# Performance work log

Measured on AMD Instinct MI355X. Metric: run time of the kernel, lower is better.

## Reference

```python
import jax, jax.numpy as jnp
import numpy as np

DIM = 1024
N_HEADS = 16
D_K = DIM // N_HEADS
B, N = 2, 2048


def _pairwise_dist(p):
    # p: [B, N, 3] -> Euclidean cdist [B, N, N], grad-safe at zero distance
    sq = jnp.sum(p * p, axis=-1)                      # [B, N]
    d2 = sq[:, :, None] + sq[:, None, :] - 2.0 * jnp.einsum('bnd,bmd->bnm', p, p)
    d2 = jnp.maximum(d2, 0.0)
    safe = jnp.where(d2 > 0.0, d2, 1.0)
    return jnp.where(d2 > 0.0, jnp.sqrt(safe), 0.0)


def setup_inputs() -> dict:
    key = jax.random.key(0)
    ks = jax.random.split(key, 11)
    s = 1.0 / np.sqrt(DIM)
    inp = {
        'x': jax.random.normal(ks[0], (B, N, DIM), jnp.float32),
        'positions': jax.random.normal(ks[1], (B, N, 3), jnp.float32),
        'W_q': jax.random.normal(ks[2], (DIM, DIM), jnp.float32) * s,
        'b_q': jnp.zeros((DIM,), jnp.float32),
        'W_k': jax.random.normal(ks[3], (DIM, DIM), jnp.float32) * s,
        'b_k': jnp.zeros((DIM,), jnp.float32),
        'W_v': jax.random.normal(ks[4], (DIM, DIM), jnp.float32) * s,
        'b_v': jnp.zeros((DIM,), jnp.float32),
        'W_o': jax.random.normal(ks[5], (DIM, DIM), jnp.float32) * s,
        'b_o': jnp.zeros((DIM,), jnp.float32),
        'dist_bias': jax.random.normal(ks[6], (N_HEADS, 1, 1), jnp.float32),
    }
    return inp


def reference(x, positions, W_q, b_q, W_k, b_k, W_v, b_v, W_o, b_o, dist_bias):
    Bv, Nv, C = x.shape
    def proj(W, b):
        # [B,N,C] -> [B,H,N,d_k]
        return (x @ W.T + b).reshape(Bv, Nv, N_HEADS, D_K).transpose(0, 2, 1, 3)
    Q = proj(W_q, b_q)
    K = proj(W_k, b_k)
    V = proj(W_v, b_v)
    attn = jnp.einsum('bhnd,bhmd->bhnm', Q, K) / np.sqrt(D_K)  # [B,H,N,N]
    dists = _pairwise_dist(positions)                          # [B,N,N]
    # log(exp(-|b|*d) + 1e-8), per-head bias broadcast over [B,H,N,N]
    dist_weights = jnp.exp(-jnp.abs(dist_bias)[None] * dists[:, None])
    attn = attn + jnp.log(dist_weights + 1e-8)
    attn = jax.nn.softmax(attn, axis=-1)
    out = jnp.einsum('bhnm,bhmd->bhnd', attn, V)               # [B,H,N,d_k]
    out = out.transpose(0, 2, 1, 3).reshape(Bv, Nv, C)
    return out @ W_o.T + b_o
```

## Files before the change

### kernel.cpp

```cpp
#include <hip/hip_runtime.h>
#include <hip/hip_bf16.h>
#include <stdint.h>

using bf16   = __hip_bfloat16;
using short8 = __attribute__((ext_vector_type(8))) short;
using f32x4  = __attribute__((ext_vector_type(4))) float;
using f32x16 = __attribute__((ext_vector_type(16))) float;

#define NSEQ   2048
#define NHEADS 16
#define DK     64
#define DMODEL 1024
#define LOG2E  1.44269504088896f

#define GLDS16(gp, lp) __builtin_amdgcn_global_load_lds( \
    (const __attribute__((address_space(1))) void*)(gp), \
    (__attribute__((address_space(3))) void*)(lp), 16, 0, 0)

__device__ __forceinline__ ushort f2bf(float f){
  bf16 h = __float2bfloat16(f);
  return __builtin_bit_cast(ushort, h);
}
__device__ __forceinline__ float bf2f(ushort u){
  uint t = ((uint)u)<<16; return __builtin_bit_cast(float, t);
}

__global__ void k_cvt_all(const float4* __restrict__ x,  const float4* __restrict__ wq,
                          const float4* __restrict__ wk, const float4* __restrict__ wv,
                          const float4* __restrict__ wo,
                          ushort4* __restrict__ xb,  ushort4* __restrict__ wqb,
                          ushort4* __restrict__ wkb, ushort4* __restrict__ wvb,
                          ushort4* __restrict__ wob){
  const int i = blockIdx.x*blockDim.x + threadIdx.x;
  const float4* s; ushort4* d; int off;
  if (i < 1048576){ s = x; d = xb; off = i; }
  else {
    const int wi = i - 1048576;
    const int w  = wi >> 18;
    off = wi & 262143;
    switch(w){
      case 0:  s = wq; d = wqb; break;
      case 1:  s = wk; d = wkb; break;
      case 2:  s = wv; d = wvb; break;
      default: s = wo; d = wob; break;
    }
  }
  float4 v = s[off];
  ushort4 o;
  o.x = f2bf(v.x); o.y = f2bf(v.y); o.z = f2bf(v.z); o.w = f2bf(v.w);
  d[off] = o;
}

__global__ void k_geo(const float* __restrict__ pos, ushort* __restrict__ AF,
                      ushort* __restrict__ BF, int n){
  int i = blockIdx.x*blockDim.x + threadIdx.x;
  if (i >= n) return;
  float x = pos[i*3+0], y = pos[i*3+1], z = pos[i*3+2];
  float sq = x*x + y*y + z*z;
  ushort xh = f2bf(x);  float xhf = bf2f(xh);  ushort xl = f2bf(x - xhf);
  ushort yh = f2bf(y);  float yhf = bf2f(yh);  ushort yl = f2bf(y - yhf);
  ushort zh = f2bf(z);  float zhf = bf2f(zh);  ushort zl = f2bf(z - zhf);
  ushort sh = f2bf(sq); float shf = bf2f(sh);  ushort sl = f2bf(sq - shf);
  ushort m2xh = f2bf(-2.f*xhf), m2xl = f2bf(-2.f*bf2f(xl));
  ushort m2yh = f2bf(-2.f*yhf), m2yl = f2bf(-2.f*bf2f(yl));
  ushort m2zh = f2bf(-2.f*zhf), m2zl = f2bf(-2.f*bf2f(zl));
  const ushort one = 0x3F80;
  ushort af[16] = {xh,xl,xh, yh,yl,yh, zh,zl,zh, sh,sl, one,one, 0,0,0};
  ushort bv[16] = {m2xh,m2xh,m2xl, m2yh,m2yh,m2yl, m2zh,m2zh,m2zl, one,one, sh,sl, 0,0,0};
  *(uint4*)&AF[i*16]     = *(uint4*)&af[0];
  *(uint4*)&AF[i*16 + 8] = *(uint4*)&af[8];
  *(uint4*)&BF[i*16]     = *(uint4*)&bv[0];
  *(uint4*)&BF[i*16 + 8] = *(uint4*)&bv[8];
}

__device__ __forceinline__ void gemm_core(
    const ushort* __restrict__ Ap, const ushort* __restrict__ Bp,
    int bm, int bn, int tid, ushort smem[2][2][4096], f32x4 (&acc)[4][4])
{
  const int wave = tid>>6, lane = tid&63;
  const int wr = wave>>1, wc = wave&1;
  const int ko   = (lane>>4)*8;
  const int srow = wave*16 + (lane>>2);
  const int scol = (lane&3)*8;

  const ushort* As = Ap + (size_t)(bm*128)*DMODEL + scol;
  const ushort* Bs = Bp + (size_t)(bn*128)*DMODEL + scol;

#define STAGEG(buf, kt) do { \
    _Pragma("unroll") \
    for (int i_=0;i_<2;i_++){ \
      GLDS16(As + (size_t)(i_*64 + srow)*DMODEL + (kt)*32, &smem[buf][0][i_*2048 + wave*512]); \
      GLDS16(Bs + (size_t)(i_*64 + srow)*DMODEL + (kt)*32, &smem[buf][1][i_*2048 + wave*512]); \
    } } while(0)

  STAGEG(0, 0);
  for (int kt=0; kt<32; ++kt){
    int cur = kt&1;
    __syncthreads();
    if (kt<31) STAGEG(cur^1, kt+1);
    short8 af[4], bfv[4];
    const ushort* At = smem[cur][0];
    const ushort* Bt = smem[cur][1];
    #pragma unroll
    for (int mi=0;mi<4;mi++) af[mi]  = *(const short8*)&At[(wr*64+mi*16+(lane&15))*32 + ko];
    #pragma unroll
    for (int ni=0;ni<4;ni++) bfv[ni] = *(const short8*)&Bt[(wc*64+ni*16+(lane&15))*32 + ko];
    #pragma unroll
    for (int mi=0;mi<4;mi++)
      #pragma unroll
      for (int ni=0;ni<4;ni++)
        acc[mi][ni] = __builtin_amdgcn_mfma_f32_16x16x32_bf16(af[mi], bfv[ni], acc[mi][ni], 0,0,0);
  }
#undef STAGEG
}

__global__ __launch_bounds__(256) void k_gemm_qkv(
    const ushort* __restrict__ xb,
    const ushort* __restrict__ Wqb, const ushort* __restrict__ Wkb, const ushort* __restrict__ Wvb,
    const float* __restrict__ bq, const float* __restrict__ bk, const float* __restrict__ bv,
    ushort* __restrict__ Qo, ushort* __restrict__ Ko, ushort* __restrict__ Vto)
{
  __shared__ ushort smem[2][2][4096];
  const int tid = threadIdx.x;
  const int work = (blockIdx.x & 7)*96 + (blockIdx.x >> 3);
  const int t = work & 255;
  const int z = work >> 8;
  const int lane = tid&63, wave = tid>>6;
  const int wr = wave>>1, wc = wave&1;

  const ushort* Ap; const ushort* Bp; const float* bias;
  ushort* outp; int bm, bn; float scale = 1.0f;
  if (z==0){ Ap=xb;  Bp=Wqb; bias=bq; outp=Qo;  bm=t>>3; bn=t&7; scale=0.125f*LOG2E; }
  else if (z==1){ Ap=xb;  Bp=Wkb; bias=bk; outp=Ko;  bm=t>>3; bn=t&7; }
  else          { Ap=Wvb; Bp=xb;  bias=bv; outp=Vto; bm=t&7;  bn=t>>3; }

  f32x4 acc[4][4] = {};
  gemm_core(Ap, Bp, bm, bn, tid, smem, acc);

  if (z<2){
    #pragma unroll
    for (int mi=0;mi<4;mi++){
      const int m0 = bm*128 + wr*64 + mi*16 + (lane>>4)*4;
      #pragma unroll
      for (int ni=0;ni<4;ni++){
        const int nn = bn*128 + wc*64 + ni*16 + (lane&15);
        const float bs = bias[nn];
        const int h = nn>>6, d = nn&63;
        #pragma unroll
        for (int j=0;j<4;j++){
          int mm = m0+j;
          int b = mm>>11, nr = mm&2047;
          size_t off = (((size_t)(b*NHEADS+h)*NSEQ) + nr)*DK + d;
          outp[off] = f2bf((acc[mi][ni][j] + bs)*scale);
        }
      }
    }
  } else {
    #pragma unroll
    for (int mi=0;mi<4;mi++){
      const int m0 = bm*128 + wr*64 + mi*16 + (lane>>4)*4;
      #pragma unroll
      for (int ni=0;ni<4;ni++){
        const int nn = bn*128 + wc*64 + ni*16 + (lane&15);
        const int b = nn>>11, nr = nn&2047;
        #pragma unroll
        for (int j=0;j<4;j++){
          int mm = m0+j;
          const float bs = bias[mm];
          int h = mm>>6, d = mm&63;
          size_t off = (((size_t)(b*NHEADS+h)*DK) + d)*NSEQ + nr;
          outp[off] = f2bf(acc[mi][ni][j] + bs);
        }
      }
    }
  }
}

__global__ __launch_bounds__(256) void k_gemm_out(
    const ushort* __restrict__ Ob, const ushort* __restrict__ Wob,
    const float* __restrict__ bo, float* __restrict__ out)
{
  __shared__ ushort smem[2][2][4096];
  const int tid = threadIdx.x;
  const int work = (blockIdx.x & 7)*32 + (blockIdx.x >> 3);
  const int lane = tid&63, wave = tid>>6;
  const int wr = wave>>1, wc = wave&1;
  const int bm = work>>3, bn = work&7;
  f32x4 acc[4][4] = {};
  gemm_core(Ob, Wob, bm, bn, tid, smem, acc);
  #pragma unroll
  for (int mi=0;mi<4;mi++){
    const int m0 = bm*128 + wr*64 + mi*16 + (lane>>4)*4;
    #pragma unroll
    for (int ni=0;ni<4;ni++){
      const int nn = bn*128 + wc*64 + ni*16 + (lane&15);
      const float bs = bo[nn];
      #pragma unroll
      for (int j=0;j<4;j++)
        out[(size_t)(m0+j)*DMODEL + nn] = acc[mi][ni][j] + bs;
    }
  }
}

__global__ __launch_bounds__(256) void k_attn(
    const ushort* __restrict__ Q, const ushort* __restrict__ K, const ushort* __restrict__ Vt,
    const ushort* __restrict__ AF, const ushort* __restrict__ BF,
    const float* __restrict__ dist_bias,
    ushort* __restrict__ O)
{
  __shared__ ushort kb[2][4096];
  __shared__ ushort vb[2][4096];
  const int tid = threadIdx.x, wave = tid>>6, lane = tid&63;
  const int work = ((blockIdx.x & 7) << 6) | (blockIdx.x >> 3);
  const int qt = work & 15, h = (work >> 4) & 15, b = work >> 8;
  const int lo5 = lane&31, hi = lane>>5;
  const float ah2 = fabsf(dist_bias[h]) * LOG2E;
  const ushort* Qh  = Q  + ((size_t)(b*NHEADS+h))*NSEQ*DK;
  const ushort* Kh  = K  + ((size_t)(b*NHEADS+h))*NSEQ*DK;
  const ushort* Vth = Vt + ((size_t)(b*NHEADS+h))*DK*NSEQ;
  const ushort* AFb = AF + (size_t)b*NSEQ*16;
  const ushort* BFb = BF + (size_t)b*NSEQ*16;

  const int q0 = qt*128 + wave*32;

  short8 qf[4];
  #pragma unroll
  for (int s=0;s<4;s++)
    qf[s] = *(const short8*)&Qh[(size_t)(q0+lo5)*DK + s*16 + hi*8];
  const short8 bfq = *(const short8*)&BFb[(size_t)(q0+lo5)*16 + hi*8];

  const int grow  = lane>>3;
  const int gc16  = (lane&7) ^ grow;
  const int rowb  = wave*8 + grow;

#define STAGE(buf, jb) do { \
    _Pragma("unroll") \
    for (int p_=0;p_<2;p_++){ \
      const int rw_ = p_*32 + rowb; \
      GLDS16(Kh  + (size_t)((jb)+rw_)*DK   + gc16*8, &kb[buf][(p_*256 + wave*64)*8]); \
      GLDS16(Vth + (size_t)rw_*NSEQ + (jb) + gc16*8, &vb[buf][(p_*256 + wave*64)*8]); \
    } } while(0)

  const int rb = lo5*64;
  const int rx = lo5 & 7;

  f32x16 o0 = {}, o1 = {};
  float l_run = 0.f;

  STAGE(0, 0);
  for (int t=0; t<32; ++t){
    const int cur = t&1;
    __syncthreads();
    if (t<31) STAGE(cur^1, (t+1)*64);
    const ushort* kbc = kb[cur];
    const ushort* vbc = vb[cur];
    #pragma unroll
    for (int ss=0; ss<2; ++ss){
      const int jb = t*64 + ss*32;
      const short8 afk = *(const short8*)&AFb[(size_t)(jb+lo5)*16 + hi*8];
      f32x16 zz = {};
      f32x16 d2 = __builtin_amdgcn_mfma_f32_32x32x16_bf16(afk, bfq, zz, 0,0,0);
      const short8 kf0 = *(const short8*)&kbc[ss*2048 + rb + (((0+hi)^rx)<<3)];
      const short8 kf1 = *(const short8*)&kbc[ss*2048 + rb + (((2+hi)^rx)<<3)];
      const short8 kf2 = *(const short8*)&kbc[ss*2048 + rb + (((4+hi)^rx)<<3)];
      const short8 kf3 = *(const short8*)&kbc[ss*2048 + rb + (((6+hi)^rx)<<3)];
      f32x16 st = {};
      st = __builtin_amdgcn_mfma_f32_32x32x16_bf16(kf0, qf[0], st, 0,0,0);
      st = __builtin_amdgcn_mfma_f32_32x32x16_bf16(kf1, qf[1], st, 0,0,0);
      st = __builtin_amdgcn_mfma_f32_32x32x16_bf16(kf2, qf[2], st, 0,0,0);
      st = __builtin_amdgcn_mfma_f32_32x32x16_bf16(kf3, qf[3], st, 0,0,0);
      float p[16];
      #pragma unroll
      for (int r=0;r<16;r++){
        float d = __builtin_amdgcn_sqrtf(fmaxf(d2[r], 0.f));
        p[r] = __builtin_exp2f(fmaf(-ah2, d, st[r]));
      }
      float s01=p[0]+p[1], s23=p[2]+p[3], s45=p[4]+p[5], s67=p[6]+p[7];
      float s89=p[8]+p[9], sab=p[10]+p[11], scd=p[12]+p[13], sef=p[14]+p[15];
      float rsum = ((s01+s23)+(s45+s67)) + ((s89+sab)+(scd+sef));
      rsum += __shfl_xor(rsum, 32);
      l_run += rsum;
      #pragma unroll
      for (int s=0;s<2;s++){
        uint w0, w1, w2, w3;
        asm("v_cvt_pk_bf16_f32 %0, %1, %2" : "=v"(w0) : "v"(p[8*s+0]), "v"(p[8*s+1]));
        asm("v_cvt_pk_bf16_f32 %0, %1, %2" : "=v"(w2) : "v"(p[8*s+4]), "v"(p[8*s+5]));
        asm("v_cvt_pk_bf16_f32 %0, %1, %2" : "=v"(w1) : "v"(p[8*s+2]), "v"(p[8*s+3]));
        asm("v_cvt_pk_bf16_f32 %0, %1, %2" : "=v"(w3) : "v"(p[8*s+6]), "v"(p[8*s+7]));
        asm volatile("v_permlane32_swap_b32 %0, %1" : "+v"(w0), "+v"(w2));
        asm volatile("v_permlane32_swap_b32 %0, %1" : "+v"(w1), "+v"(w3));
        uint4 aw; aw.x = w0; aw.y = w1; aw.z = w2; aw.w = w3;
        const short8 pa = __builtin_bit_cast(short8, aw);
        const int jcol = (ss<<2) + 2*s + hi;
        const short8 v0 = *(const short8*)&vbc[       rb + ((jcol^rx)<<3)];
        const short8 v1 = *(const short8*)&vbc[2048 + rb + ((jcol^rx)<<3)];
        o0 = __builtin_amdgcn_mfma_f32_32x32x16_bf16(pa, v0, o0, 0,0,0);
        o1 = __builtin_amdgcn_mfma_f32_32x32x16_bf16(pa, v1, o1, 0,0,0);
      }
    }
  }
#undef STAGE

  #pragma unroll
  for (int r=0;r<16;r++){
    const int src = (r&3) + 8*(r>>2) + 4*hi;
    const float lr = __shfl(l_run, src);
    const float inv = 1.f/lr;
    const int i = q0 + src;
    O[((size_t)b*NSEQ + i)*DMODEL + h*DK + lo5]      = f2bf(o0[r]*inv);
    O[((size_t)b*NSEQ + i)*DMODEL + h*DK + 32 + lo5] = f2bf(o1[r]*inv);
  }
}

extern "C" void kernel_launch(void* const* d_in, const int* in_sizes, int n_in,
                              void* d_out, int out_size, void* d_ws, size_t ws_size,
                              hipStream_t stream) {
  const float* x   = (const float*)d_in[0];
  const float* pos = (const float*)d_in[1];
  const float* Wq  = (const float*)d_in[2];
  const float* bq  = (const float*)d_in[3];
  const float* Wk  = (const float*)d_in[4];
  const float* bk  = (const float*)d_in[5];
  const float* Wv  = (const float*)d_in[6];
  const float* bv  = (const float*)d_in[7];
  const float* Wo  = (const float*)d_in[8];
  const float* bo  = (const float*)d_in[9];
  const float* db  = (const float*)d_in[10];
  float* out = (float*)d_out;

  char* ws = (char*)d_ws;
  ushort* xb   = (ushort*)(ws);
  ushort* Wqb  = (ushort*)(ws + ((size_t)8<<20));
  ushort* Wkb  = (ushort*)(ws + ((size_t)10<<20));
  ushort* Wvb  = (ushort*)(ws + ((size_t)12<<20));
  ushort* Wob  = (ushort*)(ws + ((size_t)14<<20));
  ushort* Qb   = (ushort*)(ws + ((size_t)16<<20));
  ushort* Kb   = (ushort*)(ws + ((size_t)24<<20));
  ushort* Vtb  = (ushort*)(ws + ((size_t)32<<20));
  ushort* AFt  = Wqb;
  ushort* BFt  = (ushort*)(ws + ((size_t)8<<20) + (128<<10));
  ushort* Omrg = xb;

  k_cvt_all<<<10240, 256, 0, stream>>>(
      (const float4*)x, (const float4*)Wq, (const float4*)Wk, (const float4*)Wv, (const float4*)Wo,
      (ushort4*)xb, (ushort4*)Wqb, (ushort4*)Wkb, (ushort4*)Wvb, (ushort4*)Wob);
  k_gemm_qkv<<<768, 256, 0, stream>>>(xb, Wqb, Wkb, Wvb, bq, bk, bv, Qb, Kb, Vtb);
  k_geo<<<16, 256, 0, stream>>>(pos, AFt, BFt, 2*NSEQ);
  k_attn<<<512, 256, 0, stream>>>(Qb, Kb, Vtb, AFt, BFt, db, Omrg);
  k_gemm_out<<<256, 256, 0, stream>>>(Omrg, Wob, bo, out);
}
```

Measured before the change: 243.5 us.

## Split attention key range across wave pairs and merge partial outputs via LDS

Doubles the attention block to 512 threads, with each pair of waves splitting the 2048 keys into two halves that are processed independently. The half-results are then merged through shared memory before normalisation. It also adds s_setprio around the MFMA sections and drops the XCD-swizzled block mapping in favour of a 3D grid. The intent is more waves per CU for latency hiding and a shorter serial loop per wave. In exchange it doubles LDS use, adds an LDS reduction with an extra barrier, and may lower occupancy.

```diff
diff --git a/kernel.cpp b/kernel.cpp
--- a/kernel.cpp
+++ b/kernel.cpp
@@ -202,17 +202,17 @@
   }
 }
 
-__global__ __launch_bounds__(256) void k_attn(
+__global__ __launch_bounds__(512) void k_attn(
     const ushort* __restrict__ Q, const ushort* __restrict__ K, const ushort* __restrict__ Vt,
     const ushort* __restrict__ AF, const ushort* __restrict__ BF,
     const float* __restrict__ dist_bias,
     ushort* __restrict__ O)
 {
-  __shared__ ushort kb[2][4096];
-  __shared__ ushort vb[2][4096];
+  __shared__ ushort kb[2][2][4096];
+  __shared__ ushort vb[2][2][4096];
   const int tid = threadIdx.x, wave = tid>>6, lane = tid&63;
-  const int work = ((blockIdx.x & 7) << 6) | (blockIdx.x >> 3);
-  const int qt = work & 15, h = (work >> 4) & 15, b = work >> 8;
+  const int g = wave>>1, c = wave&1;
+  const int qt = blockIdx.x, h = blockIdx.y, b = blockIdx.z;
   const int lo5 = lane&31, hi = lane>>5;
   const float ah2 = fabsf(dist_bias[h]) * LOG2E;
   const ushort* Qh  = Q  + ((size_t)(b*NHEADS+h))*NSEQ*DK;
@@ -221,7 +221,8 @@
   const ushort* AFb = AF + (size_t)b*NSEQ*16;
   const ushort* BFb = BF + (size_t)b*NSEQ*16;
 
-  const int q0 = qt*128 + wave*32;
+  const int q0 = qt*128 + g*32;
+  const int j0 = c*1024;
 
   short8 qf[4];
   #pragma unroll
@@ -231,14 +232,14 @@
 
   const int grow  = lane>>3;
   const int gc16  = (lane&7) ^ grow;
-  const int rowb  = wave*8 + grow;
+  const int rowb  = g*8 + grow;
 
 #define STAGE(buf, jb) do { \
     _Pragma("unroll") \
     for (int p_=0;p_<2;p_++){ \
       const int rw_ = p_*32 + rowb; \
-      GLDS16(Kh  + (size_t)((jb)+rw_)*DK   + gc16*8, &kb[buf][(p_*256 + wave*64)*8]); \
-      GLDS16(Vth + (size_t)rw_*NSEQ + (jb) + gc16*8, &vb[buf][(p_*256 + wave*64)*8]); \
+      GLDS16(Kh  + (size_t)((jb)+rw_)*DK   + gc16*8, &kb[buf][c][(p_*256 + g*64)*8]); \
+      GLDS16(Vth + (size_t)rw_*NSEQ + (jb) + gc16*8, &vb[buf][c][(p_*256 + g*64)*8]); \
     } } while(0)
 
   const int rb = lo5*64;
@@ -247,16 +248,16 @@
   f32x16 o0 = {}, o1 = {};
   float l_run = 0.f;
 
-  STAGE(0, 0);
-  for (int t=0; t<32; ++t){
+  STAGE(0, j0);
+  for (int t=0; t<16; ++t){
     const int cur = t&1;
     __syncthreads();
-    if (t<31) STAGE(cur^1, (t+1)*64);
-    const ushort* kbc = kb[cur];
-    const ushort* vbc = vb[cur];
+    if (t<15) STAGE(cur^1, j0 + (t+1)*64);
+    const ushort* kbc = kb[cur][c];
+    const ushort* vbc = vb[cur][c];
     #pragma unroll
     for (int ss=0; ss<2; ++ss){
-      const int jb = t*64 + ss*32;
+      const int jb = j0 + t*64 + ss*32;
       const short8 afk = *(const short8*)&AFb[(size_t)(jb+lo5)*16 + hi*8];
       f32x16 zz = {};
       f32x16 d2 = __builtin_amdgcn_mfma_f32_32x32x16_bf16(afk, bfq, zz, 0,0,0);
@@ -264,11 +265,13 @@
       const short8 kf1 = *(const short8*)&kbc[ss*2048 + rb + (((2+hi)^rx)<<3)];
       const short8 kf2 = *(const short8*)&kbc[ss*2048 + rb + (((4+hi)^rx)<<3)];
       const short8 kf3 = *(const short8*)&kbc[ss*2048 + rb + (((6+hi)^rx)<<3)];
+      __builtin_amdgcn_s_setprio(1);
       f32x16 st = {};
       st = __builtin_amdgcn_mfma_f32_32x32x16_bf16(kf0, qf[0], st, 0,0,0);
       st = __builtin_amdgcn_mfma_f32_32x32x16_bf16(kf1, qf[1], st, 0,0,0);
       st = __builtin_amdgcn_mfma_f32_32x32x16_bf16(kf2, qf[2], st, 0,0,0);
       st = __builtin_amdgcn_mfma_f32_32x32x16_bf16(kf3, qf[3], st, 0,0,0);
+      __builtin_amdgcn_s_setprio(0);
       float p[16];
       #pragma unroll
       for (int r=0;r<16;r++){
@@ -280,6 +283,7 @@
       float rsum = ((s01+s23)+(s45+s67)) + ((s89+sab)+(scd+sef));
       rsum += __shfl_xor(rsum, 32);
       l_run += rsum;
+      __builtin_amdgcn_s_setprio(1);
       #pragma unroll
       for (int s=0;s<2;s++){
         uint w0, w1, w2, w3;
@@ -297,18 +301,39 @@
         o0 = __builtin_amdgcn_mfma_f32_32x32x16_bf16(pa, v0, o0, 0,0,0);
         o1 = __builtin_amdgcn_mfma_f32_32x32x16_bf16(pa, v1, o1, 0,0,0);
       }
+      __builtin_amdgcn_s_setprio(0);
     }
   }
 #undef STAGE
 
-  #pragma unroll
-  for (int r=0;r<16;r++){
-    const int src = (r&3) + 8*(r>>2) + 4*hi;
-    const float lr = __shfl(l_run, src);
-    const float inv = 1.f/lr;
-    const int i = q0 + src;
-    O[((size_t)b*NSEQ + i)*DMODEL + h*DK + lo5]      = f2bf(o0[r]*inv);
-    O[((size_t)b*NSEQ + i)*DMODEL + h*DK + 32 + lo5] = f2bf(o1[r]*inv);
+  __syncthreads();
+  float* ms = (float*)&kb[0][0][0];
+  float* ls = (float*)&vb[0][0][0];
+  if (c == 1){
+    float* mg = ms + g*2048;
+    #pragma unroll
+    for (int k=0;k<16;k++) mg[lane*32 + ((k+lane)&31)]      = o0[k];
+    #pragma unroll
+    for (int k=0;k<16;k++) mg[lane*32 + ((16+k+lane)&31)]   = o1[k];
+    ls[g*64 + lane] = l_run;
+  }
+  __syncthreads();
+  if (c == 0){
+    const float* mg = ms + g*2048;
+    #pragma unroll
+    for (int k=0;k<16;k++) o0[k] += mg[lane*32 + ((k+lane)&31)];
+    #pragma unroll
+    for (int k=0;k<16;k++) o1[k] += mg[lane*32 + ((16+k+lane)&31)];
+    l_run += ls[g*64 + lane];
+    #pragma unroll
+    for (int r=0;r<16;r++){
+      const int src = (r&3) + 8*(r>>2) + 4*hi;
+      const float lr = __shfl(l_run, src);
+      const float inv = 1.f/lr;
+      const int i = q0 + src;
+      O[((size_t)b*NSEQ + i)*DMODEL + h*DK + lo5]      = f2bf(o0[r]*inv);
+      O[((size_t)b*NSEQ + i)*DMODEL + h*DK + 32 + lo5] = f2bf(o1[r]*inv);
+    }
   }
 }
 
@@ -346,6 +371,6 @@
       (ushort4*)xb, (ushort4*)Wqb, (ushort4*)Wkb, (ushort4*)Wvb, (ushort4*)Wob);
   k_gemm_qkv<<<768, 256, 0, stream>>>(xb, Wqb, Wkb, Wvb, bq, bk, bv, Qb, Kb, Vtb);
   k_geo<<<16, 256, 0, stream>>>(pos, AFt, BFt, 2*NSEQ);
-  k_attn<<<512, 256, 0, stream>>>(Qb, Kb, Vtb, AFt, BFt, db, Omrg);
+  k_attn<<<dim3(16,NHEADS,2), 512, 0, stream>>>(Qb, Kb, Vtb, AFt, BFt, db, Omrg);
   k_gemm_out<<<256, 256, 0, stream>>>(Omrg, Wob, bo, out);
 }
```

Measured after the change: 248.1 us. No clear change (+1.9%).
